# Optimization experiments

Hardware: AMD Instinct MI355X
Metric: run time of the kernel (lower is better)

Reference implementation:

```python
import jax, jax.numpy as jnp
import numpy as np

B, S, HID = 2, 2048, 2048
NH = 16
Q_LORA, KV_LORA = 1024, 512
NOPE, ROPE, VD = 128, 64, 128
QK = NOPE + ROPE  # 192
EPS = 1e-6
THETA = 10000.0


def rms_norm(x, w, eps=EPS):
    x32 = x.astype(jnp.float32)
    var = jnp.mean(x32 * x32, axis=-1, keepdims=True)
    return (w * (x32 * jax.lax.rsqrt(var + eps))).astype(x.dtype)


def rotate_half(x):
    h = x.shape[-1] // 2
    return jnp.concatenate([-x[..., h:], x[..., :h]], axis=-1)


def setup_inputs() -> dict:
    key = jax.random.key(0)
    ks = jax.random.split(key, 8)
    hidden_states = jax.random.normal(ks[0], (B, S, HID), dtype=jnp.float32)
    attention_mask = jnp.zeros((B, 1, 1, S), dtype=jnp.float32)
    # RoPE tables (true rotary values)
    inv_freq = 1.0 / (THETA ** (np.arange(0, ROPE, 2, dtype=np.float32) / ROPE))
    pos = np.arange(S, dtype=np.float32)
    freqs = np.outer(pos, inv_freq)  # [S, ROPE/2]
    emb = np.concatenate([freqs, freqs], axis=-1)  # [S, ROPE]
    cos = jnp.asarray(np.cos(emb), dtype=jnp.float32)
    sin = jnp.asarray(np.sin(emb), dtype=jnp.float32)
    # Parameters, stored as [in, out] so y = x @ W
    sd = lambda fan_in: 1.0 / np.sqrt(fan_in)
    w_q_down = jax.random.normal(ks[1], (HID, Q_LORA), dtype=jnp.float32) * sd(HID)
    w_q_up = jax.random.normal(ks[2], (Q_LORA, NH * QK), dtype=jnp.float32) * sd(Q_LORA)
    w_kv_down = jax.random.normal(ks[3], (HID, KV_LORA + ROPE), dtype=jnp.float32) * sd(HID)
    w_kv_up = jax.random.normal(ks[4], (KV_LORA, NH * (NOPE + VD)), dtype=jnp.float32) * sd(KV_LORA)
    w_o = jax.random.normal(ks[5], (NH * VD, HID), dtype=jnp.float32) * sd(NH * VD)
    q_norm_w = jnp.ones((Q_LORA,), dtype=jnp.float32)
    kv_norm_w = jnp.ones((KV_LORA,), dtype=jnp.float32)
    return dict(hidden_states=hidden_states, attention_mask=attention_mask,
                cos=cos, sin=sin, w_q_down=w_q_down, w_q_up=w_q_up,
                w_kv_down=w_kv_down, w_kv_up=w_kv_up, w_o=w_o,
                q_norm_w=q_norm_w, kv_norm_w=kv_norm_w)


def reference(hidden_states, attention_mask, cos, sin,
              w_q_down, w_q_up, w_kv_down, w_kv_up, w_o,
              q_norm_w, kv_norm_w):
    b, s, _ = hidden_states.shape
    # --- Q path: down-proj -> RMSNorm -> up-proj ---
    q = rms_norm(hidden_states @ w_q_down, q_norm_w) @ w_q_up  # [b,s,NH*QK]
    q = q.reshape(b, s, NH, QK).transpose(0, 2, 1, 3)          # [b,h,s,QK]
    q_nope, q_rope = q[..., :NOPE], q[..., NOPE:]
    # --- KV path: down-proj -> split latent / rope key -> up-proj ---
    kv = hidden_states @ w_kv_down                              # [b,s,KV_LORA+ROPE]
    kv_latent, k_rope = kv[..., :KV_LORA], kv[..., KV_LORA:]
    kv_up = rms_norm(kv_latent, kv_norm_w) @ w_kv_up            # [b,s,NH*(NOPE+VD)]
    kv_up = kv_up.reshape(b, s, NH, NOPE + VD).transpose(0, 2, 1, 3)
    k_nope, v = kv_up[..., :NOPE], kv_up[..., NOPE:]            # [b,h,s,*]
    k_rope = k_rope[:, None, :, :]                              # [b,1,s,ROPE] (broadcast over heads)
    # --- partial RoPE ---
    c = cos[None, None, :, :]
    sn = sin[None, None, :, :]
    q_rope = q_rope * c + rotate_half(q_rope) * sn
    k_rope = k_rope * c + rotate_half(k_rope) * sn
    q_final = jnp.concatenate([q_nope, q_rope], axis=-1)        # [b,h,s,QK]
    k_final = jnp.concatenate([k_nope, jnp.broadcast_to(k_rope, (b, NH, s, ROPE))], axis=-1)
    # --- SDPA (non-causal, additive mask) ---
    scale = 1.0 / jnp.sqrt(jnp.asarray(QK, dtype=jnp.float32))
    scores = jnp.einsum('bhqd,bhkd->bhqk', q_final, k_final) * scale
    scores = scores + attention_mask                            # [b,1,1,s] broadcast
    probs = jax.nn.softmax(scores.astype(jnp.float32), axis=-1).astype(q_final.dtype)
    attn = jnp.einsum('bhqk,bhkd->bhqd', probs, v)              # [b,h,s,VD]
    attn = attn.transpose(0, 2, 1, 3).reshape(b, s, NH * VD)
    return attn @ w_o
```

## Files before the change

kernel.cpp:

```cpp
#include <hip/hip_runtime.h>
#include <hip/hip_bf16.h>

typedef unsigned short u16;
typedef unsigned int u32;
typedef short s16x8 __attribute__((ext_vector_type(8)));
typedef float f32x4 __attribute__((ext_vector_type(4)));
typedef float f32x2 __attribute__((ext_vector_type(2)));

__device__ __forceinline__ float bf2f(u16 u) {
    union { u32 i; float f; } v; v.i = ((u32)u) << 16; return v.f;
}
__device__ __forceinline__ u16 f2bf(float f) {
    union { float f; u32 i; } v; v.f = f;
    u32 i = v.i;
    u32 r = (i + 0x7FFFu + ((i >> 16) & 1u)) >> 16;
    return (u16)r;
}

__device__ __forceinline__ void gl2lds16(const u16* g, u16* l) {
    __builtin_amdgcn_global_load_lds(
        (const __attribute__((address_space(1))) u32*)g,
        (__attribute__((address_space(3))) u32*)l, 16, 0, 0);
}

__global__ __launch_bounds__(256) void cvt_f32_bf16(
    const float* __restrict__ in, u16* __restrict__ out, long long n2)
{
    long long i = (long long)blockIdx.x * 256 + threadIdx.x;
    if (i < n2) {
        f32x2 v = *(const f32x2*)(in + i * 2);
        u32 p = (u32)f2bf(v[0]) | ((u32)f2bf(v[1]) << 16);
        *(u32*)(out + i * 2) = p;
    }
}

__global__ __launch_bounds__(256) void transpose_f32_bf16(
    const float* __restrict__ in, u16* __restrict__ out, int R, int C)
{
    __shared__ u16 t[32][33];
    int tx = threadIdx.x & 31, ty = threadIdx.x >> 5;
    int c0 = blockIdx.x * 32, r0 = blockIdx.y * 32;
    #pragma unroll
    for (int i = 0; i < 32; i += 8)
        t[ty + i][tx] = f2bf(in[(size_t)(r0 + ty + i) * C + c0 + tx]);
    __syncthreads();
    #pragma unroll
    for (int i = 0; i < 32; i += 8)
        out[(size_t)(c0 + ty + i) * R + r0 + tx] = t[tx][ty + i];
}

__global__ __launch_bounds__(256) void transpose_v(
    const u16* __restrict__ kvup, u16* __restrict__ vt)
{
    __shared__ u16 t[32][33];
    int tx = threadIdx.x & 31, ty = threadIdx.x >> 5;
    int s0 = blockIdx.x * 32, v0 = blockIdx.y * 32;
    int b = blockIdx.z >> 4, h = blockIdx.z & 15;
    #pragma unroll
    for (int i = 0; i < 32; i += 8)
        t[ty + i][tx] = kvup[(size_t)(b * 2048 + s0 + ty + i) * 4096 + h * 256 + 128 + v0 + tx];
    __syncthreads();
    #pragma unroll
    for (int i = 0; i < 32; i += 8)
        vt[((size_t)(b * 16 + h) * 128 + v0 + ty + i) * 2048 + s0 + tx] = t[tx][ty + i];
}

__global__ __launch_bounds__(256) void gemm_bf16(
    const u16* __restrict__ A, const u16* __restrict__ Bt, u16* __restrict__ C,
    int M, int N, int K)
{
    __shared__ u16 As[64][40];
    __shared__ u16 Bs[64][40];

    const int tid  = threadIdx.x;
    const int wave = tid >> 6, lane = tid & 63;
    const int quad = lane >> 4, l16 = lane & 15;
    const int m0 = blockIdx.y * 64, n0 = blockIdx.x * 64;
    const int wm = (wave >> 1) * 32, wn = (wave & 1) * 32;

    const int srow = tid >> 2;
    const int koff = (tid & 3) * 8;

    f32x4 acc00 = {0.f,0.f,0.f,0.f};
    f32x4 acc01 = {0.f,0.f,0.f,0.f};
    f32x4 acc10 = {0.f,0.f,0.f,0.f};
    f32x4 acc11 = {0.f,0.f,0.f,0.f};

    for (int k0 = 0; k0 < K; k0 += 32) {
        *(s16x8*)&As[srow][koff] = *(const s16x8*)&A[(size_t)(m0 + srow) * K + k0 + koff];
        *(s16x8*)&Bs[srow][koff] = *(const s16x8*)&Bt[(size_t)(n0 + srow) * K + k0 + koff];
        __syncthreads();
        s16x8 a0 = *(const s16x8*)&As[wm + l16][quad * 8];
        s16x8 a1 = *(const s16x8*)&As[wm + 16 + l16][quad * 8];
        s16x8 b0 = *(const s16x8*)&Bs[wn + l16][quad * 8];
        s16x8 b1 = *(const s16x8*)&Bs[wn + 16 + l16][quad * 8];
        acc00 = __builtin_amdgcn_mfma_f32_16x16x32_bf16(a0, b0, acc00, 0, 0, 0);
        acc01 = __builtin_amdgcn_mfma_f32_16x16x32_bf16(a0, b1, acc01, 0, 0, 0);
        acc10 = __builtin_amdgcn_mfma_f32_16x16x32_bf16(a1, b0, acc10, 0, 0, 0);
        acc11 = __builtin_amdgcn_mfma_f32_16x16x32_bf16(a1, b1, acc11, 0, 0, 0);
        __syncthreads();
    }

    #pragma unroll
    for (int r = 0; r < 4; ++r) {
        int row0 = m0 + wm + quad * 4 + r;
        int col0 = n0 + wn + l16;
        C[(size_t)row0 * N + col0]             = f2bf(acc00[r]);
        C[(size_t)row0 * N + col0 + 16]        = f2bf(acc01[r]);
        C[(size_t)(row0 + 16) * N + col0]      = f2bf(acc10[r]);
        C[(size_t)(row0 + 16) * N + col0 + 16] = f2bf(acc11[r]);
    }
}

template <typename OUT>
__global__ __launch_bounds__(256) void gemm128(
    const u16* __restrict__ A, const u16* __restrict__ Bt, OUT* __restrict__ C,
    int M, int N, int K)
{
    __shared__ u16 As[128 * 32];
    __shared__ u16 Bs[128 * 32];

    const int tid  = threadIdx.x;
    const int wave = tid >> 6, lane = tid & 63;
    const int quad = lane >> 4, l16 = lane & 15;
    const int m0 = blockIdx.y * 128, n0 = blockIdx.x * 128;
    const int wm = (wave >> 1) * 64, wn = (wave & 1) * 64;

    const int srow = lane >> 2, soct = (lane & 3) * 8;

    f32x4 acc[4][4];
    #pragma unroll
    for (int i = 0; i < 4; ++i)
        #pragma unroll
        for (int j = 0; j < 4; ++j) acc[i][j] = (f32x4){0.f,0.f,0.f,0.f};

    for (int k0 = 0; k0 < K; k0 += 32) {
        #pragma unroll
        for (int op = 0; op < 2; ++op) {
            int g = wave * 2 + op;
            gl2lds16(&A[(size_t)(m0 + g * 16 + srow) * K + k0 + soct], &As[g * 512]);
            gl2lds16(&Bt[(size_t)(n0 + g * 16 + srow) * K + k0 + soct], &Bs[g * 512]);
        }
        __syncthreads();
        s16x8 af[4], bf[4];
        #pragma unroll
        for (int i = 0; i < 4; ++i) {
            af[i] = *(const s16x8*)&As[(wm + i * 16 + l16) * 32 + quad * 8];
            bf[i] = *(const s16x8*)&Bs[(wn + i * 16 + l16) * 32 + quad * 8];
        }
        #pragma unroll
        for (int i = 0; i < 4; ++i)
            #pragma unroll
            for (int j = 0; j < 4; ++j)
                acc[i][j] = __builtin_amdgcn_mfma_f32_16x16x32_bf16(af[i], bf[j], acc[i][j], 0, 0, 0);
        __syncthreads();
    }

    #pragma unroll
    for (int i = 0; i < 4; ++i) {
        #pragma unroll
        for (int j = 0; j < 4; ++j) {
            #pragma unroll
            for (int r = 0; r < 4; ++r) {
                int row = m0 + wm + i * 16 + quad * 4 + r;
                int col = n0 + wn + j * 16 + l16;
                if constexpr (sizeof(OUT) == 2)
                    C[(size_t)row * N + col] = f2bf(acc[i][j][r]);
                else
                    C[(size_t)row * N + col] = acc[i][j][r];
            }
        }
    }
}

__global__ __launch_bounds__(256) void rmsnorm_kernel(
    const u16* __restrict__ in, const float* __restrict__ w, u16* __restrict__ out,
    int len, int istride, int ostride)
{
    const int row = blockIdx.x, tid = threadIdx.x;
    const u16* x = in + (size_t)row * istride;
    float ss = 0.f;
    for (int i = tid; i < len; i += 256) { float v = bf2f(x[i]); ss += v * v; }
    #pragma unroll
    for (int off = 32; off >= 1; off >>= 1) ss += __shfl_xor(ss, off, 64);
    __shared__ float wsum[4];
    if ((tid & 63) == 0) wsum[tid >> 6] = ss;
    __syncthreads();
    float tot = wsum[0] + wsum[1] + wsum[2] + wsum[3];
    float inv = 1.0f / sqrtf(tot / (float)len + 1e-6f);
    for (int i = tid; i < len; i += 256) {
        float v = bf2f(x[i]);
        out[(size_t)row * ostride + i] = f2bf(v * inv * w[i]);
    }
}

__global__ __launch_bounds__(256) void rope_kernel(
    u16* __restrict__ qb, const u16* __restrict__ kvb, u16* __restrict__ krot,
    const float* __restrict__ cosb, const float* __restrict__ sinb)
{
    const int row = blockIdx.x;
    const int s = row & 2047;
    const int lane = threadIdx.x & 63, wave = threadIdx.x >> 6;
    const float c  = cosb[s * 64 + lane];
    const float sn = sinb[s * 64 + lane];
    for (int seg = wave; seg < 17; seg += 4) {
        const u16* pin; u16* pout;
        if (seg < 16) { pout = qb + (size_t)row * 3072 + seg * 192 + 128; pin = pout; }
        else          { pin = kvb + (size_t)row * 576 + 512; pout = krot + (size_t)row * 64; }
        float x  = bf2f(pin[lane]);
        float xp = bf2f(pin[lane ^ 32]);
        float rot = (lane < 32) ? -xp : xp;
        pout[lane] = f2bf(x * c + rot * sn);
    }
}

__global__ __launch_bounds__(256, 2) void attn_mfma9(
    const u16* __restrict__ qb,
    const u16* __restrict__ kvup,
    const u16* __restrict__ krot,
    const u16* __restrict__ vt,
    const float* __restrict__ mask,
    u16* __restrict__ attnb)
{
    __shared__ u16 Ks[64 * 200];
    __shared__ u16 Ps[128 * 72];
    __shared__ u16 Vd[2][128 * 64];

    const int tid  = threadIdx.x;
    const int wave = tid >> 6, lane = tid & 63;
    const int quad = lane >> 4, l16 = lane & 15;
    const int qt = blockIdx.x, h = blockIdx.y, b = blockIdx.z;
    const int row0 = b * 2048 + qt * 128;
    const int qw = wave * 16;
    const float scale2 = 0.10411610f;
    const float l2e    = 1.4426950408889634f;
    const int swz = (l16 & 7) << 3;

    s16x8 onesf;
    #pragma unroll
    for (int j = 0; j < 8; ++j) onesf[j] = (short)0x3F80;

    s16x8 qf[2][6];
    #pragma unroll
    for (int s = 0; s < 2; ++s)
        #pragma unroll
        for (int kc = 0; kc < 6; ++kc)
            qf[s][kc] = *(const s16x8*)&qb[(size_t)(row0 + s * 64 + qw + l16) * 3072
                                           + h * 192 + kc * 32 + quad * 8];

    const u16* pk[6]; int offk[6], stepk[6];
    #pragma unroll
    for (int i = 0; i < 6; ++i) {
        int idx = tid + i * 256;
        int r = idx / 24, c = (idx % 24) * 8;
        offk[i] = r * 200 + c;
        if (c < 128) { pk[i] = kvup + (size_t)(b * 2048 + r) * 4096 + h * 256 + c; stepk[i] = 64 * 4096; }
        else         { pk[i] = krot + (size_t)(b * 2048 + r) * 64 + (c - 128);     stepk[i] = 64 * 64;   }
    }

    const u16* vtb = vt + (size_t)(b * 16 + h) * 128 * 2048;
    const u16* pv[4];
    #pragma unroll
    for (int i = 0; i < 4; ++i) {
        int widx = i * 4 + wave;
        int r = widx * 8 + (lane >> 3);
        int u = (lane & 7) ^ (lane >> 3);
        pv[i] = vtb + (size_t)r * 2048 + u * 8;
    }

    s16x8 kreg[6];
    #pragma unroll
    for (int i = 0; i < 6; ++i) { kreg[i] = *(const s16x8*)pk[i]; pk[i] += stepk[i]; }
    #pragma unroll
    for (int i = 0; i < 4; ++i) {
        gl2lds16(pv[i], &Vd[0][(i * 4 + wave) * 512]);
        pv[i] += 64;
    }

    float m = -__builtin_inff();
    f32x4 l[2] = {(f32x4){0.f,0.f,0.f,0.f}, (f32x4){0.f,0.f,0.f,0.f}};
    f32x4 O[2][8];
    #pragma unroll
    for (int s = 0; s < 2; ++s)
        #pragma unroll
        for (int vi = 0; vi < 8; ++vi) O[s][vi] = (f32x4){0.f,0.f,0.f,0.f};

    for (int kt = 0; kt < 32; ++kt) {
        __syncthreads();
        #pragma unroll
        for (int i = 0; i < 6; ++i) *(s16x8*)&Ks[offk[i]] = kreg[i];
        __syncthreads();

        if (kt < 31) {
            #pragma unroll
            for (int i = 0; i < 6; ++i) { kreg[i] = *(const s16x8*)pk[i]; pk[i] += stepk[i]; }
            #pragma unroll
            for (int i = 0; i < 4; ++i) {
                gl2lds16(pv[i], &Vd[(kt + 1) & 1][(i * 4 + wave) * 512]);
                pv[i] += 64;
            }
        }
        float mv4[4];
        #pragma unroll
        for (int ct = 0; ct < 4; ++ct)
            mv4[ct] = mask[b * 2048 + kt * 64 + ct * 16 + l16] * l2e;

        f32x4 S[2][4];
        #pragma unroll
        for (int s = 0; s < 2; ++s)
            #pragma unroll
            for (int ct = 0; ct < 4; ++ct) S[s][ct] = (f32x4){0.f,0.f,0.f,0.f};
        __builtin_amdgcn_s_setprio(1);
        #pragma unroll
        for (int kc = 0; kc < 6; ++kc) {
            #pragma unroll
            for (int ct = 0; ct < 4; ++ct) {
                s16x8 bfr = *(const s16x8*)&Ks[(ct * 16 + l16) * 200 + kc * 32 + quad * 8];
                S[0][ct] = __builtin_amdgcn_mfma_f32_16x16x32_bf16(qf[0][kc], bfr, S[0][ct], 0, 0, 0);
                S[1][ct] = __builtin_amdgcn_mfma_f32_16x16x32_bf16(qf[1][kc], bfr, S[1][ct], 0, 0, 0);
            }
        }
        __builtin_amdgcn_s_setprio(0);

        #pragma unroll
        for (int ct = 0; ct < 4; ++ct)
            #pragma unroll
            for (int s = 0; s < 2; ++s)
                #pragma unroll
                for (int r = 0; r < 4; ++r) S[s][ct][r] = S[s][ct][r] * scale2 + mv4[ct];

        float tm = S[0][0][0];
        #pragma unroll
        for (int s = 0; s < 2; ++s)
            #pragma unroll
            for (int ct = 0; ct < 4; ++ct)
                #pragma unroll
                for (int r = 0; r < 4; ++r) tm = fmaxf(tm, S[s][ct][r]);

        if (!__all(tm <= m + 8.0f)) {
            #pragma unroll
            for (int off = 1; off < 64; off <<= 1)
                tm = fmaxf(tm, __shfl_xor(tm, off, 64));
            float mn = fmaxf(m, tm);
            float alpha = exp2f(m - mn);
            m = mn;
            #pragma unroll
            for (int s = 0; s < 2; ++s) {
                l[s] *= alpha;
                #pragma unroll
                for (int vi = 0; vi < 8; ++vi) O[s][vi] *= alpha;
            }
        }

        #pragma unroll
        for (int s = 0; s < 2; ++s)
            #pragma unroll
            for (int ct = 0; ct < 4; ++ct)
                #pragma unroll
                for (int r = 0; r < 4; ++r)
                    Ps[(s * 64 + qw + quad * 4 + r) * 72 + ct * 16 + l16]
                        = f2bf(exp2f(S[s][ct][r] - m));

        const u16* Vb = Vd[kt & 1];
        __builtin_amdgcn_s_setprio(1);
        #pragma unroll
        for (int kc = 0; kc < 2; ++kc) {
            s16x8 a0 = *(const s16x8*)&Ps[(qw + l16) * 72 + kc * 32 + quad * 8];
            s16x8 a1 = *(const s16x8*)&Ps[(64 + qw + l16) * 72 + kc * 32 + quad * 8];
            #pragma unroll
            for (int vi = 0; vi < 8; ++vi) {
                int rowv = vi * 16 + l16;
                int col  = kc * 32 + quad * 8;
                s16x8 bfr = *(const s16x8*)&Vb[rowv * 64 + (col ^ swz)];
                O[0][vi] = __builtin_amdgcn_mfma_f32_16x16x32_bf16(a0, bfr, O[0][vi], 0, 0, 0);
                O[1][vi] = __builtin_amdgcn_mfma_f32_16x16x32_bf16(a1, bfr, O[1][vi], 0, 0, 0);
            }
            l[0] = __builtin_amdgcn_mfma_f32_16x16x32_bf16(a0, onesf, l[0], 0, 0, 0);
            l[1] = __builtin_amdgcn_mfma_f32_16x16x32_bf16(a1, onesf, l[1], 0, 0, 0);
        }
        __builtin_amdgcn_s_setprio(0);
    }

    #pragma unroll
    for (int s = 0; s < 2; ++s) {
        f32x4 linv;
        #pragma unroll
        for (int r = 0; r < 4; ++r) linv[r] = 1.0f / l[s][r];
        #pragma unroll
        for (int vi = 0; vi < 8; ++vi) {
            #pragma unroll
            for (int r = 0; r < 4; ++r) {
                int q_ = row0 + s * 64 + qw + quad * 4 + r;
                attnb[(size_t)q_ * 2048 + h * 128 + vi * 16 + l16] = f2bf(O[s][vi][r] * linv[r]);
            }
        }
    }
}

extern "C" void kernel_launch(void* const* d_in, const int* in_sizes, int n_in,
                              void* d_out, int out_size, void* d_ws, size_t ws_size,
                              hipStream_t stream)
{
    const float* hidden = (const float*)d_in[0];
    const float* mask   = (const float*)d_in[1];
    const float* cosb   = (const float*)d_in[2];
    const float* sinb   = (const float*)d_in[3];
    const float* w_qd   = (const float*)d_in[4];
    const float* w_qu   = (const float*)d_in[5];
    const float* w_kvd  = (const float*)d_in[6];
    const float* w_kvu  = (const float*)d_in[7];
    const float* w_o    = (const float*)d_in[8];
    const float* qnw    = (const float*)d_in[9];
    const float* kvnw   = (const float*)d_in[10];
    float* out = (float*)d_out;

    u16* ws = (u16*)d_ws;
    u16* qbuf   = ws + 0;
    u16* wt_qd  = ws + 0;
    u16* kvup   = ws + 12582912;
    u16* hid_bf = ws + 12582912;
    u16* wt_kvd = ws + 20971520;
    u16* attnb  = ws + 29360128;
    u16* qd     = ws + 29360128;
    u16* wt_qu  = ws + 33554432;
    u16* kvb    = ws + 37748736;
    u16* wt_o   = ws + 37748736;
    u16* kvn    = ws + 40108032;
    u16* wt_kvu = ws + 42205184;
    u16* krot   = ws + 44302336;
    u16* vt     = ws + 44564480;

    {
        long long n2 = (long long)4096 * 2048 / 2;
        cvt_f32_bf16<<<(int)((n2 + 255) / 256), 256, 0, stream>>>(hidden, hid_bf, n2);
    }

    transpose_f32_bf16<<<dim3(32, 64), 256, 0, stream>>>(w_qd, wt_qd, 2048, 1024);
    gemm128<u16><<<dim3(8, 32), 256, 0, stream>>>(hid_bf, wt_qd, qd, 4096, 1024, 2048);
    rmsnorm_kernel<<<4096, 256, 0, stream>>>(qd, qnw, qd, 1024, 1024, 1024);
    transpose_f32_bf16<<<dim3(96, 32), 256, 0, stream>>>(w_qu, wt_qu, 1024, 3072);
    gemm128<u16><<<dim3(24, 32), 256, 0, stream>>>(qd, wt_qu, qbuf, 4096, 3072, 1024);

    transpose_f32_bf16<<<dim3(18, 64), 256, 0, stream>>>(w_kvd, wt_kvd, 2048, 576);
    gemm_bf16<<<dim3(9, 64), 256, 0, stream>>>(hid_bf, wt_kvd, kvb, 4096, 576, 2048);
    rmsnorm_kernel<<<4096, 256, 0, stream>>>(kvb, kvnw, kvn, 512, 576, 512);
    transpose_f32_bf16<<<dim3(128, 16), 256, 0, stream>>>(w_kvu, wt_kvu, 512, 4096);
    gemm128<u16><<<dim3(32, 32), 256, 0, stream>>>(kvn, wt_kvu, kvup, 4096, 4096, 512);

    transpose_v<<<dim3(64, 4, 32), 256, 0, stream>>>(kvup, vt);

    rope_kernel<<<4096, 256, 0, stream>>>(qbuf, kvb, krot, cosb, sinb);
    transpose_f32_bf16<<<dim3(64, 64), 256, 0, stream>>>(w_o, wt_o, 2048, 2048);

    attn_mfma9<<<dim3(16, 16, 2), 256, 0, stream>>>(qbuf, kvup, krot, vt, mask, attnb);

    gemm128<float><<<dim3(16, 32), 256, 0, stream>>>(attnb, wt_o, out, 4096, 2048, 2048);
}
```

Baseline: 511.5 us.

## Read K/V fragments directly from global memory and remap blocks per XCD

The attention kernel drops its LDS staging of K and V tiles, along with the register prefetch and the barriers around it. Each wave now loads its MFMA B-fragments straight from global memory and relies on L2 to hold them. The launch becomes a 1D grid that is remapped so the 16 query tiles of each (batch, head) pair land on the same XCD, which is meant to improve L2 reuse of that head's K and V. The cost is that every wave issues redundant global loads with no software prefetch, so load latency is exposed directly to the MFMA loop.

```diff
diff --git a/kernel.cpp b/kernel.cpp
--- a/kernel.cpp
+++ b/kernel.cpp
@@ -214,7 +214,7 @@
     }
 }
 
-__global__ __launch_bounds__(256, 2) void attn_mfma9(
+__global__ __launch_bounds__(256, 2) void attn_mfma10(
     const u16* __restrict__ qb,
     const u16* __restrict__ kvup,
     const u16* __restrict__ krot,
@@ -222,19 +222,22 @@
     const float* __restrict__ mask,
     u16* __restrict__ attnb)
 {
-    __shared__ u16 Ks[64 * 200];
     __shared__ u16 Ps[128 * 72];
-    __shared__ u16 Vd[2][128 * 64];
 
     const int tid  = threadIdx.x;
     const int wave = tid >> 6, lane = tid & 63;
     const int quad = lane >> 4, l16 = lane & 15;
-    const int qt = blockIdx.x, h = blockIdx.y, b = blockIdx.z;
+
+    const int bid  = blockIdx.x;
+    const int xcd  = bid & 7, slot = bid >> 3;
+    const int pair = xcd * 4 + (slot >> 4);
+    const int qt   = slot & 15;
+    const int h    = pair & 15, b = pair >> 4;
+
     const int row0 = b * 2048 + qt * 128;
     const int qw = wave * 16;
     const float scale2 = 0.10411610f;
     const float l2e    = 1.4426950408889634f;
-    const int swz = (l16 & 7) << 3;
 
     s16x8 onesf;
     #pragma unroll
@@ -248,34 +251,9 @@
             qf[s][kc] = *(const s16x8*)&qb[(size_t)(row0 + s * 64 + qw + l16) * 3072
                                            + h * 192 + kc * 32 + quad * 8];
 
-    const u16* pk[6]; int offk[6], stepk[6];
-    #pragma unroll
-    for (int i = 0; i < 6; ++i) {
-        int idx = tid + i * 256;
-        int r = idx / 24, c = (idx % 24) * 8;
-        offk[i] = r * 200 + c;
-        if (c < 128) { pk[i] = kvup + (size_t)(b * 2048 + r) * 4096 + h * 256 + c; stepk[i] = 64 * 4096; }
-        else         { pk[i] = krot + (size_t)(b * 2048 + r) * 64 + (c - 128);     stepk[i] = 64 * 64;   }
-    }
-
-    const u16* vtb = vt + (size_t)(b * 16 + h) * 128 * 2048;
-    const u16* pv[4];
-    #pragma unroll
-    for (int i = 0; i < 4; ++i) {
-        int widx = i * 4 + wave;
-        int r = widx * 8 + (lane >> 3);
-        int u = (lane & 7) ^ (lane >> 3);
-        pv[i] = vtb + (size_t)r * 2048 + u * 8;
-    }
-
-    s16x8 kreg[6];
-    #pragma unroll
-    for (int i = 0; i < 6; ++i) { kreg[i] = *(const s16x8*)pk[i]; pk[i] += stepk[i]; }
-    #pragma unroll
-    for (int i = 0; i < 4; ++i) {
-        gl2lds16(pv[i], &Vd[0][(i * 4 + wave) * 512]);
-        pv[i] += 64;
-    }
+    const u16* kb_n = kvup + (size_t)(b * 2048) * 4096 + h * 256;
+    const u16* kb_r = krot + (size_t)(b * 2048) * 64;
+    const u16* vtb  = vt + (size_t)(b * 16 + h) * 128 * 2048;
 
     float m = -__builtin_inff();
     f32x4 l[2] = {(f32x4){0.f,0.f,0.f,0.f}, (f32x4){0.f,0.f,0.f,0.f}};
@@ -286,20 +264,6 @@
         for (int vi = 0; vi < 8; ++vi) O[s][vi] = (f32x4){0.f,0.f,0.f,0.f};
 
     for (int kt = 0; kt < 32; ++kt) {
-        __syncthreads();
-        #pragma unroll
-        for (int i = 0; i < 6; ++i) *(s16x8*)&Ks[offk[i]] = kreg[i];
-        __syncthreads();
-
-        if (kt < 31) {
-            #pragma unroll
-            for (int i = 0; i < 6; ++i) { kreg[i] = *(const s16x8*)pk[i]; pk[i] += stepk[i]; }
-            #pragma unroll
-            for (int i = 0; i < 4; ++i) {
-                gl2lds16(pv[i], &Vd[(kt + 1) & 1][(i * 4 + wave) * 512]);
-                pv[i] += 64;
-            }
-        }
         float mv4[4];
         #pragma unroll
         for (int ct = 0; ct < 4; ++ct)
@@ -315,7 +279,11 @@
         for (int kc = 0; kc < 6; ++kc) {
             #pragma unroll
             for (int ct = 0; ct < 4; ++ct) {
-                s16x8 bfr = *(const s16x8*)&Ks[(ct * 16 + l16) * 200 + kc * 32 + quad * 8];
+                int krow = kt * 64 + ct * 16 + l16;
+                const u16* src = (kc < 4)
+                    ? &kb_n[(size_t)krow * 4096 + kc * 32 + quad * 8]
+                    : &kb_r[(size_t)krow * 64 + (kc - 4) * 32 + quad * 8];
+                s16x8 bfr = *(const s16x8*)src;
                 S[0][ct] = __builtin_amdgcn_mfma_f32_16x16x32_bf16(qf[0][kc], bfr, S[0][ct], 0, 0, 0);
                 S[1][ct] = __builtin_amdgcn_mfma_f32_16x16x32_bf16(qf[1][kc], bfr, S[1][ct], 0, 0, 0);
             }
@@ -361,7 +329,6 @@
                     Ps[(s * 64 + qw + quad * 4 + r) * 72 + ct * 16 + l16]
                         = f2bf(exp2f(S[s][ct][r] - m));
 
-        const u16* Vb = Vd[kt & 1];
         __builtin_amdgcn_s_setprio(1);
         #pragma unroll
         for (int kc = 0; kc < 2; ++kc) {
@@ -369,9 +336,8 @@
             s16x8 a1 = *(const s16x8*)&Ps[(64 + qw + l16) * 72 + kc * 32 + quad * 8];
             #pragma unroll
             for (int vi = 0; vi < 8; ++vi) {
-                int rowv = vi * 16 + l16;
-                int col  = kc * 32 + quad * 8;
-                s16x8 bfr = *(const s16x8*)&Vb[rowv * 64 + (col ^ swz)];
+                s16x8 bfr = *(const s16x8*)&vtb[(size_t)(vi * 16 + l16) * 2048
+                                                + kt * 64 + kc * 32 + quad * 8];
                 O[0][vi] = __builtin_amdgcn_mfma_f32_16x16x32_bf16(a0, bfr, O[0][vi], 0, 0, 0);
                 O[1][vi] = __builtin_amdgcn_mfma_f32_16x16x32_bf16(a1, bfr, O[1][vi], 0, 0, 0);
             }
@@ -452,7 +418,7 @@
     rope_kernel<<<4096, 256, 0, stream>>>(qbuf, kvb, krot, cosb, sinb);
     transpose_f32_bf16<<<dim3(64, 64), 256, 0, stream>>>(w_o, wt_o, 2048, 2048);
 
-    attn_mfma9<<<dim3(16, 16, 2), 256, 0, stream>>>(qbuf, kvup, krot, vt, mask, attnb);
+    attn_mfma10<<<512, 256, 0, stream>>>(qbuf, kvup, krot, vt, mask, attnb);
 
     gemm128<float><<<dim3(16, 32), 256, 0, stream>>>(attnb, wt_o, out, 4096, 2048, 2048);
 }
```

Measured after the change: 671.6 us. 31.3% more time.
